# Kernel tuning notes

Hardware: AMD Instinct MI355X
Metric: run time of the kernel (lower is better)

The kernel has to match this reference:

```python
import jax, jax.numpy as jnp
import numpy as np


def _quat_to_rotT(q):
    # q: [..., 4] in (w, x, y, z) order, exactly mirroring the torch entry order,
    # including the final transpose(3, 2). Returns [..., 3, 3].
    w, x, y, z = q[..., 0], q[..., 1], q[..., 2], q[..., 3]
    R = jnp.stack([
        1.0 - 2.0 * (y ** 2 + z ** 2), 2.0 * x * y - 2.0 * w * z, 2.0 * w * y + 2.0 * x * z,
        2.0 * x * y + 2.0 * z * w, 1.0 - 2.0 * (x ** 2 + z ** 2), -2.0 * w * x + 2.0 * y * z,
        -2.0 * w * y + 2.0 * x * z, 2.0 * w * x + 2.0 * y * z, 1.0 - 2.0 * (x ** 2 + y ** 2),
    ], axis=-1).reshape(q.shape[:-1] + (3, 3))
    return jnp.swapaxes(R, -1, -2)


def _forward(pred_t, pred_r, pred_c, target_r, target_t, model_points, choose, symmetric, diameters, rot_anchors):
    bs, num_rot, _ = pred_r.shape
    # --- anchor regularization: cos_dist = bmm(pred_r, rot_anchors^T) ---
    cos_dist = jnp.einsum('brq,aq->bra', pred_r, rot_anchors)  # [bs, R, R]
    diag = jnp.diagonal(cos_dist, axis1=1, axis2=2)             # [bs, R]
    reg = jnp.max(cos_dist, axis=2) - diag
    loss_reg = jnp.mean(jnp.where(reg > 0.001, reg, 0.0))       # F.threshold(x, 0.001, 0)

    # --- rotate model points by every anchor-refined rotation ---
    rotT = _quat_to_rotT(pred_r)                                 # [bs, R, 3, 3]
    mp = model_points[:, 0]                                      # [bs, N, 3]
    pred_pts = jnp.einsum('bnk,brkj->brnj', mp, rotT)            # [bs, R, N, 3]
    tgt = target_r[:, 0]                                         # [bs, M, 3]

    # symmetric branch: pairwise distances via the |a|^2+|b|^2-2ab expansion
    # (avoids materializing the [bs,R,N,M,3] difference tensor; dist tensor only)
    a2 = jnp.sum(pred_pts ** 2, axis=-1)                         # [bs, R, N]
    b2 = jnp.sum(tgt ** 2, axis=-1)                              # [bs, M]
    ab = jnp.einsum('brnk,bmk->brnm', pred_pts, tgt)             # [bs, R, N, M]
    d2 = a2[:, :, :, None] + b2[:, None, None, :] - 2.0 * ab
    dist_pair = jnp.sqrt(jnp.maximum(d2, 1e-12))
    sym_d = jnp.mean(jnp.min(dist_pair, axis=3), axis=2)         # [bs, R]

    # non-symmetric branch: pointwise distance (M == N)
    nonsym_d = jnp.mean(
        jnp.linalg.norm(pred_pts - tgt[:, None, :, :], axis=-1), axis=2)  # [bs, R]

    d = jnp.where(symmetric[:, None], sym_d, nonsym_d)           # [bs, R]
    per_anchor = d / (diameters[:, None] * pred_c) + jnp.log(pred_c)
    loss_r = jnp.sum(jnp.mean(per_anchor, axis=1))               # summed over batch (torch +=)

    # --- translation smooth-L1 against sampled dense field ---
    tflat = jnp.transpose(target_t, (0, 2, 3, 1)).reshape(bs, -1, 3)      # [bs, H*W, 3]
    tsamp = jnp.take_along_axis(tflat, choose[:, :, None], axis=1)        # [bs, n_sel, 3]
    diff_t = pred_t - tsamp
    ad = jnp.abs(diff_t)
    loss_t = jnp.mean(jnp.where(ad < 1.0, 0.5 * diff_t ** 2, ad - 0.5))

    total = loss_r + 2.0 * loss_reg + 5.0 * loss_t
    return total, loss_r, loss_reg, loss_t


def setup_inputs() -> dict:
    key = jax.random.key(0)
    ks = jax.random.split(key, 8)
    bs, num_rot, N, H, W = 8, 60, 500, 80, 80
    pred_t = jax.random.normal(ks[0], (bs, N, 3), jnp.float32)
    pred_r = jax.random.normal(ks[1], (bs, num_rot, 4), jnp.float32)
    pred_c = jax.random.uniform(ks[2], (bs, num_rot), jnp.float32, 0.05, 1.0)
    target_r = jax.random.normal(ks[3], (bs, 1, N, 3), jnp.float32)
    target_t = jax.random.normal(ks[4], (bs, 3, H, W), jnp.float32)
    model_points = jax.random.normal(ks[5], (bs, 1, N, 3), jnp.float32)
    choose = jax.random.randint(ks[6], (bs, N), 0, H * W)
    symmetric = jnp.ones((bs,), dtype=bool)
    diameters = jnp.ones((bs,), jnp.float32)
    rot_anchors = jax.random.normal(ks[7], (num_rot, 4), jnp.float32)
    return {
        'pred_t': pred_t, 'pred_r': pred_r, 'pred_c': pred_c,
        'target_r': target_r, 'target_t': target_t, 'model_points': model_points,
        'choose': choose, 'symmetric': symmetric, 'diameters': diameters,
        'rot_anchors': rot_anchors,
    }


def reference(pred_t, pred_r, pred_c, target_r, target_t, model_points, choose, symmetric, diameters, rot_anchors):
    return _forward(pred_t, pred_r, pred_c, target_r, target_t, model_points,
                    choose, symmetric, diameters, rot_anchors)
```

## Files before the change

### kernel.cpp

```cpp
#include <hip/hip_runtime.h>
#include <math.h>

#define BS 8
#define NR 60
#define NRP 30
#define NP 500
#define NHW 6400
#define NPAIR (BS*NR)
#define NBLK (BS*NRP)
#define NT_ELEMS (BS*NP*3)
#define LT_PER_BLK 50

#define BIGF 3.4e38f

__global__ __launch_bounds__(512) void main_kernel(
    const float* __restrict__ pred_t,
    const float* __restrict__ pred_r,
    const float* __restrict__ target_r,
    const float* __restrict__ target_t,
    const float* __restrict__ model_points,
    const int*   __restrict__ choose,
    const float* __restrict__ rot_anchors,
    float* __restrict__ out_sym,
    float* __restrict__ out_non,
    float* __restrict__ out_reg,
    float* __restrict__ out_lt)
{
    const int bid = blockIdx.x;
    const int b  = bid / NRP;
    const int rp = bid % NRP;
    const int r0 = 2 * rp, r1 = 2 * rp + 1;
    const int pair0 = b * NR + r0;
    const int tid = threadIdx.x;
    const int wv = tid >> 6;
    const int ln = tid & 63;

    __shared__ float4 t4s[NP];
    __shared__ float2 part2[8 * 8 * 64];

    if (tid < NP) {
        const float* p = target_r + (b * NP + tid) * 3;
        float x = p[0], y = p[1], z = p[2];
        t4s[tid] = make_float4(x, y, z, x * x + y * y + z * z);
    }

    const float* q0p = pred_r + pair0 * 4;
    const float w0 = q0p[0], x0 = q0p[1], y0 = q0p[2], z0 = q0p[3];
    const float w1 = q0p[4], x1 = q0p[5], y1 = q0p[6], z1 = q0p[7];

    const float A00 = 1.f - 2.f * (y0 * y0 + z0 * z0);
    const float A01 = 2.f * x0 * y0 - 2.f * w0 * z0;
    const float A02 = 2.f * w0 * y0 + 2.f * x0 * z0;
    const float A10 = 2.f * x0 * y0 + 2.f * z0 * w0;
    const float A11 = 1.f - 2.f * (x0 * x0 + z0 * z0);
    const float A12 = -2.f * w0 * x0 + 2.f * y0 * z0;
    const float A20 = -2.f * w0 * y0 + 2.f * x0 * z0;
    const float A21 = 2.f * w0 * x0 + 2.f * y0 * z0;
    const float A22 = 1.f - 2.f * (x0 * x0 + y0 * y0);

    const float B00 = 1.f - 2.f * (y1 * y1 + z1 * z1);
    const float B01 = 2.f * x1 * y1 - 2.f * w1 * z1;
    const float B02 = 2.f * w1 * y1 + 2.f * x1 * z1;
    const float B10 = 2.f * x1 * y1 + 2.f * z1 * w1;
    const float B11 = 1.f - 2.f * (x1 * x1 + z1 * z1);
    const float B12 = -2.f * w1 * x1 + 2.f * y1 * z1;
    const float B20 = -2.f * w1 * y1 + 2.f * x1 * z1;
    const float B21 = 2.f * w1 * x1 + 2.f * y1 * z1;
    const float B22 = 1.f - 2.f * (x1 * x1 + y1 * y1);

    float lt = 0.f;
    if (tid < LT_PER_BLK) {
        int e = bid * LT_PER_BLK + tid;
        int bb = e / 1500;
        int rem = e - bb * 1500;
        int n = rem / 3;
        int k = rem - n * 3;
        int pos = choose[bb * NP + n];
        float ts = target_t[(bb * 3 + k) * NHW + pos];
        float diff = pred_t[e] - ts;
        float ad = fabsf(diff);
        lt = (ad < 1.f) ? 0.5f * diff * diff : ad - 0.5f;
    }

    if (tid < 64) {
        float dot = -BIGF;
        if (tid < NR) {
            const float* an = rot_anchors + tid * 4;
            dot = w0 * an[0] + x0 * an[1] + y0 * an[2] + z0 * an[3];
        }
        float diag = __shfl(dot, r0, 64);
        float mx = dot;
        for (int o = 32; o > 0; o >>= 1) mx = fmaxf(mx, __shfl_down(mx, o, 64));
        for (int o = 32; o > 0; o >>= 1) lt += __shfl_down(lt, o, 64);
        if (tid == 0) {
            float rg = mx - diag;
            out_reg[pair0] = (rg > 0.001f) ? rg : 0.f;
            out_lt[bid] = lt;
        }
    } else if (tid < 128) {
        float dot = -BIGF;
        if (ln < NR) {
            const float* an = rot_anchors + ln * 4;
            dot = w1 * an[0] + x1 * an[1] + y1 * an[2] + z1 * an[3];
        }
        float diag = __shfl(dot, r1, 64);
        float mx = dot;
        for (int o = 32; o > 0; o >>= 1) mx = fmaxf(mx, __shfl_down(mx, o, 64));
        if (ln == 0) {
            float rg = mx - diag;
            out_reg[pair0 + 1] = (rg > 0.001f) ? rg : 0.f;
        }
    }

    float nAx[8], nAy[8], nAz[8], nBx[8], nBy[8], nBz[8];
    const float* mpb = model_points + b * NP * 3;
#pragma unroll
    for (int k = 0; k < 8; ++k) {
        int pt = k * 64 + ln;
        int pc = (pt < NP) ? pt : 0;
        float mx_ = mpb[pc * 3 + 0], my_ = mpb[pc * 3 + 1], mz_ = mpb[pc * 3 + 2];
        float pax = A00 * mx_ + A01 * my_ + A02 * mz_;
        float pay = A10 * mx_ + A11 * my_ + A12 * mz_;
        float paz = A20 * mx_ + A21 * my_ + A22 * mz_;
        float pbx = B00 * mx_ + B01 * my_ + B02 * mz_;
        float pby = B10 * mx_ + B11 * my_ + B12 * mz_;
        float pbz = B20 * mx_ + B21 * my_ + B22 * mz_;
        nAx[k] = -2.f * pax; nAy[k] = -2.f * pay; nAz[k] = -2.f * paz;
        nBx[k] = -2.f * pbx; nBy[k] = -2.f * pby; nBz[k] = -2.f * pbz;
    }

    __syncthreads();

    const int mstart = (wv * NP) >> 3;
    const int mend   = ((wv + 1) * NP) >> 3;
    float mnA[8], mnB[8];
#pragma unroll
    for (int k = 0; k < 8; ++k) { mnA[k] = BIGF; mnB[k] = BIGF; }

    for (int m = mstart; m < mend; ++m) {
        float4 t = t4s[m];
#pragma unroll
        for (int k = 0; k < 8; ++k) {
            float dA = fmaf(nAx[k], t.x, fmaf(nAy[k], t.y, fmaf(nAz[k], t.z, t.w)));
            mnA[k] = fminf(mnA[k], dA);
            float dB = fmaf(nBx[k], t.x, fmaf(nBy[k], t.y, fmaf(nBz[k], t.z, t.w)));
            mnB[k] = fminf(mnB[k], dB);
        }
    }

#pragma unroll
    for (int k = 0; k < 8; ++k)
        part2[(wv * 8 + k) * 64 + ln] = make_float2(mnA[k], mnB[k]);
    __syncthreads();

    if (wv < 2) {
        const float* partf = (const float*)part2;
        float symsum = 0.f, nonsum = 0.f;
#pragma unroll
        for (int k = 0; k < 8; ++k) {
            float mn = BIGF;
#pragma unroll
            for (int w2 = 0; w2 < 8; ++w2) {
                float v = partf[((w2 * 8 + k) * 64 + ln) * 2 + wv];
                mn = fminf(mn, v);
            }
            float px = -0.5f * ((wv == 0) ? nAx[k] : nBx[k]);
            float py = -0.5f * ((wv == 0) ? nAy[k] : nBy[k]);
            float pz = -0.5f * ((wv == 0) ? nAz[k] : nBz[k]);
            float a2 = px * px + py * py + pz * pz;
            int pt = k * 64 + ln;
            if (pt < NP) {
                float d2 = fmaxf(a2 + mn, 1e-12f);
                symsum += sqrtf(d2);
                float4 t = t4s[pt];
                float dx = px - t.x, dy = py - t.y, dz = pz - t.z;
                nonsum += sqrtf(dx * dx + dy * dy + dz * dz);
            }
        }
        for (int o = 32; o > 0; o >>= 1) {
            symsum += __shfl_down(symsum, o, 64);
            nonsum += __shfl_down(nonsum, o, 64);
        }
        if (ln == 0) {
            out_sym[pair0 + wv] = symsum;
            out_non[pair0 + wv] = nonsum;
        }
    }
}

__global__ __launch_bounds__(256) void finalize_kernel(
    const float* __restrict__ out_sym, const float* __restrict__ out_non,
    const float* __restrict__ out_reg, const float* __restrict__ out_lt,
    const float* __restrict__ pred_c,
    const unsigned char* __restrict__ symU8, const int* __restrict__ symI,
    const float* __restrict__ diam, float* __restrict__ out)
{
    const int tid = threadIdx.x;
    float s_r = 0.f, s_reg = 0.f, s_t = 0.f;
    for (int i = tid; i < NPAIR; i += 256) {
        int b = i / NR;
        bool sym = (symU8[b] != 0) || (symI[b] != 0);
        float sum = sym ? out_sym[i] : out_non[i];
        float d = sum * (1.0f / NP);
        float c = pred_c[i];
        s_r += (d / (diam[b] * c) + logf(c)) * (1.0f / NR);
        s_reg += out_reg[i];
        if (i < NBLK) s_t += out_lt[i];
    }
    __shared__ float red[12];
    for (int o = 32; o > 0; o >>= 1) {
        s_r += __shfl_down(s_r, o, 64);
        s_reg += __shfl_down(s_reg, o, 64);
        s_t += __shfl_down(s_t, o, 64);
    }
    const int wv = tid >> 6, ln = tid & 63;
    if (ln == 0) { red[wv] = s_r; red[4 + wv] = s_reg; red[8 + wv] = s_t; }
    __syncthreads();
    if (tid == 0) {
        float lr = red[0] + red[1] + red[2] + red[3];
        float lreg = (red[4] + red[5] + red[6] + red[7]) * (1.0f / NPAIR);
        float ltv = (red[8] + red[9] + red[10] + red[11]) * (1.0f / NT_ELEMS);
        out[0] = lr + 2.f * lreg + 5.f * ltv;
        out[1] = lr;
        out[2] = lreg;
        out[3] = ltv;
    }
}

extern "C" void kernel_launch(void* const* d_in, const int* in_sizes, int n_in,
                              void* d_out, int out_size, void* d_ws, size_t ws_size,
                              hipStream_t stream) {
    const float* pred_t       = (const float*)d_in[0];
    const float* pred_r       = (const float*)d_in[1];
    const float* pred_c       = (const float*)d_in[2];
    const float* target_r     = (const float*)d_in[3];
    const float* target_t     = (const float*)d_in[4];
    const float* model_points = (const float*)d_in[5];
    const int*   choose       = (const int*)d_in[6];
    const unsigned char* symU8 = (const unsigned char*)d_in[7];
    const int*   symI         = (const int*)d_in[7];
    const float* diam         = (const float*)d_in[8];
    const float* anchors      = (const float*)d_in[9];
    float* out = (float*)d_out;

    char* ws = (char*)d_ws;
    float* o_sym = (float*)ws;
    float* o_non = o_sym + NPAIR;
    float* o_reg = o_non + NPAIR;
    float* o_lt  = o_reg + NPAIR;

    main_kernel<<<NBLK, 512, 0, stream>>>(pred_t, pred_r, target_r, target_t,
                                          model_points, choose, anchors,
                                          o_sym, o_non, o_reg, o_lt);
    finalize_kernel<<<1, 256, 0, stream>>>(o_sym, o_non, o_reg, o_lt,
                                           pred_c, symU8, symI, diam, out);
}
```

Before: 91.78 us.

## Fuse finalize into main kernel via last-block atomic counter; unroll min loop

Removes the separate finalize launch. Each block bumps a global counter, and the last block to finish does the final reduction, after a threadfence so the other blocks' partial results are visible. The inner min loop is unrolled by two target points for more instruction-level parallelism. The non-symmetric distance is now computed only when the object is not symmetric. The counter is never reset but uses modulo NBLK, so it stays correct across repeated calls, at the cost of extra fences and an atomic per block.

```diff
diff --git a/kernel.cpp b/kernel.cpp
--- a/kernel.cpp
+++ b/kernel.cpp
@@ -13,6 +13,8 @@
 
 #define BIGF 3.4e38f
 
+__device__ unsigned int g_ctr = 0u;
+
 __global__ __launch_bounds__(512) void main_kernel(
     const float* __restrict__ pred_t,
     const float* __restrict__ pred_r,
@@ -21,10 +23,15 @@
     const float* __restrict__ model_points,
     const int*   __restrict__ choose,
     const float* __restrict__ rot_anchors,
+    const float* __restrict__ pred_c,
+    const unsigned char* __restrict__ symU8,
+    const int*   __restrict__ symI,
+    const float* __restrict__ diam,
     float* __restrict__ out_sym,
     float* __restrict__ out_non,
     float* __restrict__ out_reg,
-    float* __restrict__ out_lt)
+    float* __restrict__ out_lt,
+    float* __restrict__ out)
 {
     const int bid = blockIdx.x;
     const int b  = bid / NRP;
@@ -37,6 +44,9 @@
 
     __shared__ float4 t4s[NP];
     __shared__ float2 part2[8 * 8 * 64];
+    __shared__ unsigned int s_last;
+
+    const bool symb = (symU8[b] != 0) || (symI[b] != 0);
 
     if (tid < NP) {
         const float* p = target_r + (b * NP + tid) * 3;
@@ -137,7 +147,21 @@
 #pragma unroll
     for (int k = 0; k < 8; ++k) { mnA[k] = BIGF; mnB[k] = BIGF; }
 
-    for (int m = mstart; m < mend; ++m) {
+    int m = mstart;
+    for (; m + 1 < mend; m += 2) {
+        float4 t0 = t4s[m];
+        float4 t1 = t4s[m + 1];
+#pragma unroll
+        for (int k = 0; k < 8; ++k) {
+            float dA0 = fmaf(nAx[k], t0.x, fmaf(nAy[k], t0.y, fmaf(nAz[k], t0.z, t0.w)));
+            float dA1 = fmaf(nAx[k], t1.x, fmaf(nAy[k], t1.y, fmaf(nAz[k], t1.z, t1.w)));
+            mnA[k] = fminf(mnA[k], fminf(dA0, dA1));
+            float dB0 = fmaf(nBx[k], t0.x, fmaf(nBy[k], t0.y, fmaf(nBz[k], t0.z, t0.w)));
+            float dB1 = fmaf(nBx[k], t1.x, fmaf(nBy[k], t1.y, fmaf(nBz[k], t1.z, t1.w)));
+            mnB[k] = fminf(mnB[k], fminf(dB0, dB1));
+        }
+    }
+    if (m < mend) {
         float4 t = t4s[m];
 #pragma unroll
         for (int k = 0; k < 8; ++k) {
@@ -172,9 +196,11 @@
             if (pt < NP) {
                 float d2 = fmaxf(a2 + mn, 1e-12f);
                 symsum += sqrtf(d2);
-                float4 t = t4s[pt];
-                float dx = px - t.x, dy = py - t.y, dz = pz - t.z;
-                nonsum += sqrtf(dx * dx + dy * dy + dz * dz);
+                if (!symb) {
+                    float4 t = t4s[pt];
+                    float dx = px - t.x, dy = py - t.y, dz = pz - t.z;
+                    nonsum += sqrtf(dx * dx + dy * dy + dz * dz);
+                }
             }
         }
         for (int o = 32; o > 0; o >>= 1) {
@@ -183,43 +209,48 @@
         }
         if (ln == 0) {
             out_sym[pair0 + wv] = symsum;
-            out_non[pair0 + wv] = nonsum;
-        }
-    }
-}
-
-__global__ __launch_bounds__(256) void finalize_kernel(
-    const float* __restrict__ out_sym, const float* __restrict__ out_non,
-    const float* __restrict__ out_reg, const float* __restrict__ out_lt,
-    const float* __restrict__ pred_c,
-    const unsigned char* __restrict__ symU8, const int* __restrict__ symI,
-    const float* __restrict__ diam, float* __restrict__ out)
-{
-    const int tid = threadIdx.x;
+            if (!symb) out_non[pair0 + wv] = nonsum;
+        }
+    }
+
+    __syncthreads();
+    if (tid == 0) {
+        __threadfence();
+        unsigned int old = atomicAdd(&g_ctr, 1u);
+        s_last = ((old % NBLK) == (NBLK - 1)) ? 1u : 0u;
+    }
+    __syncthreads();
+    if (s_last == 0u) return;
+
+    __threadfence();
     float s_r = 0.f, s_reg = 0.f, s_t = 0.f;
-    for (int i = tid; i < NPAIR; i += 256) {
-        int b = i / NR;
-        bool sym = (symU8[b] != 0) || (symI[b] != 0);
-        float sum = sym ? out_sym[i] : out_non[i];
-        float d = sum * (1.0f / NP);
-        float c = pred_c[i];
-        s_r += (d / (diam[b] * c) + logf(c)) * (1.0f / NR);
-        s_reg += out_reg[i];
-        if (i < NBLK) s_t += out_lt[i];
-    }
-    __shared__ float red[12];
+    if (tid < NPAIR) {
+        int bb2 = tid / NR;
+        bool sym2 = (symU8[bb2] != 0) || (symI[bb2] != 0);
+        float sum = sym2 ? out_sym[tid] : out_non[tid];
+        float dd = sum * (1.0f / NP);
+        float c = pred_c[tid];
+        s_r = (dd / (diam[bb2] * c) + logf(c)) * (1.0f / NR);
+        s_reg = out_reg[tid];
+    }
+    if (tid < NBLK) s_t = out_lt[tid];
+
     for (int o = 32; o > 0; o >>= 1) {
-        s_r += __shfl_down(s_r, o, 64);
+        s_r  += __shfl_down(s_r, o, 64);
         s_reg += __shfl_down(s_reg, o, 64);
-        s_t += __shfl_down(s_t, o, 64);
-    }
-    const int wv = tid >> 6, ln = tid & 63;
-    if (ln == 0) { red[wv] = s_r; red[4 + wv] = s_reg; red[8 + wv] = s_t; }
+        s_t  += __shfl_down(s_t, o, 64);
+    }
+    float* red = (float*)part2;
+    if (ln == 0) { red[wv] = s_r; red[8 + wv] = s_reg; red[16 + wv] = s_t; }
     __syncthreads();
     if (tid == 0) {
-        float lr = red[0] + red[1] + red[2] + red[3];
-        float lreg = (red[4] + red[5] + red[6] + red[7]) * (1.0f / NPAIR);
-        float ltv = (red[8] + red[9] + red[10] + red[11]) * (1.0f / NT_ELEMS);
+        float lr = 0.f, lreg = 0.f, ltv = 0.f;
+#pragma unroll
+        for (int w2 = 0; w2 < 8; ++w2) {
+            lr += red[w2]; lreg += red[8 + w2]; ltv += red[16 + w2];
+        }
+        lreg *= (1.0f / NPAIR);
+        ltv  *= (1.0f / NT_ELEMS);
         out[0] = lr + 2.f * lreg + 5.f * ltv;
         out[1] = lr;
         out[2] = lreg;
@@ -251,7 +282,6 @@
 
     main_kernel<<<NBLK, 512, 0, stream>>>(pred_t, pred_r, target_r, target_t,
                                           model_points, choose, anchors,
-                                          o_sym, o_non, o_reg, o_lt);
-    finalize_kernel<<<1, 256, 0, stream>>>(o_sym, o_non, o_reg, o_lt,
-                                           pred_c, symU8, symI, diam, out);
+                                          pred_c, symU8, symI, diam,
+                                          o_sym, o_non, o_reg, o_lt, out);
 }
```

Result: no change. 92.25 us (+0.5%).
